# Kernel optimization log

Measured on AMD Instinct MI355X. Metric: run time of the kernel, lower is better.

Reference implementation:

```python
import jax, jax.numpy as jnp
import numpy as np

WS = (8, 8, 8)          # window_size (d, h, w) -- all equal
N_TOK = WS[0] * WS[1] * WS[2]   # 512
DIM = 192
HEADS = 6
HEAD_DIM = DIM // HEADS  # 32
B_ = 64                  # num_windows * batch (batch = 1)


def _build_rel_coords_table():
    # matches torch: meshgrid of arange(-(w-1), w) per axis, normalized, *8, signed log2
    r = np.arange(-(WS[0] - 1), WS[0], dtype=np.float32)
    tab = np.stack(np.meshgrid(r, r, r, indexing='ij'), axis=-1)[None]  # (1,15,15,15,3)
    tab = tab / (WS[0] - 1)
    tab = tab * 8.0
    tab = np.sign(tab) * np.log2(np.abs(tab) + 1.0) / np.log2(8.0)
    return tab.astype(np.float32)


def _build_rel_pos_index():
    c = np.arange(WS[0])
    coords = np.stack(np.meshgrid(c, c, c, indexing='ij'))          # (3, 8, 8, 8)
    flat = coords.reshape(3, -1)                                     # (3, N)
    rel = flat[:, :, None] - flat[:, None, :]                        # (3, N, N)
    rel = rel.transpose(1, 2, 0).copy()                              # (N, N, 3)
    rel += WS[0] - 1
    rel[:, :, 0] *= (2 * WS[1] - 1) * (2 * WS[2] - 1)
    rel[:, :, 1] *= 2 * WS[2] - 1
    return rel.sum(-1).astype(np.int32)                              # (N, N)


def setup_inputs() -> dict:
    key = jax.random.key(0)
    ks = jax.random.split(key, 8)
    x = jax.random.normal(ks[0], (B_, N_TOK, DIM), dtype=jnp.float32)
    # 0 / -inf style additive mask (use large negative finite for stability)
    m = jax.random.uniform(ks[1], (B_, N_TOK, N_TOK))
    mask = jnp.where(m < 0.1, jnp.float32(-1e4), jnp.float32(0.0))
    w_qkv = jax.random.normal(ks[2], (3 * DIM, DIM), dtype=jnp.float32) * (DIM ** -0.5)
    q_bias = jnp.zeros((DIM,), jnp.float32)
    v_bias = jnp.zeros((DIM,), jnp.float32)
    cpb_w1 = jax.random.normal(ks[3], (512, 3), dtype=jnp.float32) * 0.3
    cpb_b1 = jnp.zeros((512,), jnp.float32)
    cpb_w2 = jax.random.normal(ks[4], (HEADS, 512), dtype=jnp.float32) * 0.05
    rel_coords_table = jnp.asarray(_build_rel_coords_table())
    rel_pos_index = jnp.asarray(_build_rel_pos_index())
    return {"x": x, "mask": mask, "w_qkv": w_qkv, "q_bias": q_bias,
            "v_bias": v_bias, "cpb_w1": cpb_w1, "cpb_b1": cpb_b1,
            "cpb_w2": cpb_w2, "rel_coords_table": rel_coords_table,
            "rel_pos_index": rel_pos_index}


def reference(x, mask, w_qkv, q_bias, v_bias, cpb_w1, cpb_b1, cpb_w2,
              rel_coords_table, rel_pos_index):
    Bw, N, C = x.shape
    H, D = HEADS, HEAD_DIM
    # qkv projection with bias = cat(q_bias, zeros, v_bias)
    qkv_bias = jnp.concatenate([q_bias, jnp.zeros_like(v_bias), v_bias])
    qkv = x @ w_qkv.T + qkv_bias                       # (Bw, N, 3C)
    qkv = qkv.reshape(Bw, N, 3, H, D).transpose(2, 0, 3, 1, 4)
    q, k, v = qkv[0], qkv[1], qkv[2]                   # (Bw, H, N, D)
    # continuous position bias MLP: 3 -> 512 -> H
    tab = rel_coords_table.reshape(-1, 3)              # (3375, 3)
    tab = jax.nn.relu(tab @ cpb_w1.T + cpb_b1) @ cpb_w2.T  # (3375, H)
    bias = tab[rel_pos_index.reshape(-1)].reshape(N, N, H)
    bias = 16.0 * jax.nn.sigmoid(bias.transpose(2, 0, 1))  # (H, N, N)
    # SDPA with additive mask (standard 1/sqrt(D) scaling, as in forward_flash)
    scale = jnp.float32(1.0 / np.sqrt(D))
    scores = jnp.einsum('bhnd,bhmd->bhnm', q, k) * scale
    scores = scores + mask[:, None, :, :] + bias[None]
    attn = jax.nn.softmax(scores, axis=-1)
    out = jnp.einsum('bhnm,bhmd->bhnd', attn, v)       # (Bw, H, N, D)
    return out
```

## Files before the change

kernel.cpp:

```cpp
#include <hip/hip_runtime.h>
#include <hip/hip_bf16.h>


typedef __bf16 bf16x8 __attribute__((ext_vector_type(8)));
typedef __bf16 bf16x4v __attribute__((ext_vector_type(4)));
typedef float  f32x4  __attribute__((ext_vector_type(4)));
typedef _Float16 f16x4 __attribute__((ext_vector_type(4)));
typedef _Float16 f16x8 __attribute__((ext_vector_type(8)));
typedef unsigned uint2v __attribute__((ext_vector_type(2)));
typedef int int4v __attribute__((ext_vector_type(4)));
typedef unsigned long long u64;

#define LOG2E 1.4426950408889634f

__device__ __forceinline__ bf16x8 cvt2_bf16x8(f32x4 a, f32x4 b) {
  bf16x8 r;
  r[0] = (__bf16)a[0]; r[1] = (__bf16)a[1]; r[2] = (__bf16)a[2]; r[3] = (__bf16)a[3];
  r[4] = (__bf16)b[0]; r[5] = (__bf16)b[1]; r[6] = (__bf16)b[2]; r[7] = (__bf16)b[3];
  return r;
}

__device__ __forceinline__ unsigned pack2bf(float a, float b) {
  unsigned short ua = __builtin_bit_cast(unsigned short, (__bf16)a);
  unsigned short ub = __builtin_bit_cast(unsigned short, (__bf16)b);
  return (unsigned)ua | ((unsigned)ub << 16);
}

__device__ __forceinline__ bf16x8 frag_from_words(unsigned w0, unsigned w1,
                                                  unsigned w2, unsigned w3) {
  union { unsigned u[4]; bf16x8 v; } f;
  f.u[0] = w0; f.u[1] = w1; f.u[2] = w2; f.u[3] = w3;
  return f.v;
}

#define PREP_MB    2048
#define PREP_WCONV 108
#define PREP_CPB   3375
#define PREP_GRID  (PREP_MB + PREP_WCONV + PREP_CPB)

__global__ __launch_bounds__(256) void prep_kernel(
    const float* __restrict__ w, __bf16* __restrict__ wbf,
    const float* __restrict__ table, const float* __restrict__ w1,
    const float* __restrict__ b1, const float* __restrict__ w2,
    float* __restrict__ tab6,
    const float* __restrict__ m, u64* __restrict__ bits)
{
  __shared__ float red[4][6];
  int blk = blockIdx.x;
  if (blk < PREP_MB) {
    int li8 = threadIdx.x & 7;
    for (size_t t = (size_t)blk * 256 + threadIdx.x;
         t < 2097152ull; t += (size_t)PREP_MB * 256) {
      const float* mp = m + t * 8;
      f32x4 v0 = *(const f32x4*)mp;
      f32x4 v1 = *(const f32x4*)(mp + 4);
      unsigned byte =
          (v0[0] == 0.f ? 1u : 0u)  | (v0[1] == 0.f ? 2u : 0u) |
          (v0[2] == 0.f ? 4u : 0u)  | (v0[3] == 0.f ? 8u : 0u) |
          (v1[0] == 0.f ? 16u : 0u) | (v1[1] == 0.f ? 32u : 0u) |
          (v1[2] == 0.f ? 64u : 0u) | (v1[3] == 0.f ? 128u : 0u);
      u64 part = (u64)byte << (8 * li8);
      part |= __shfl_xor(part, 1);
      part |= __shfl_xor(part, 2);
      part |= __shfl_xor(part, 4);
      if (li8 == 0) {
        int w_ = (int)(t >> 3);
        int b = w_ >> 12, i = (w_ >> 3) & 511, jw = w_ & 7;
        bits[(((size_t)b * 8 + jw) << 9) + i] = part;
      }
    }
  } else if (blk < PREP_MB + PREP_WCONV) {
    int t = (blk - PREP_MB) * 256 + threadIdx.x;
    f32x4 v = *(const f32x4*)(w + (size_t)t * 4);
    bf16x4v o;
    o[0] = (__bf16)v[0]; o[1] = (__bf16)v[1]; o[2] = (__bf16)v[2]; o[3] = (__bf16)v[3];
    *(bf16x4v*)(wbf + (size_t)t * 4) = o;
  } else {
    int p = blk - PREP_MB - PREP_WCONV;
    float c0 = table[p * 3 + 0], c1 = table[p * 3 + 1], c2 = table[p * 3 + 2];
    float acc[6] = {0.f, 0.f, 0.f, 0.f, 0.f, 0.f};
#pragma unroll
    for (int jj = 0; jj < 2; ++jj) {
      int j = threadIdx.x + jj * 256;
      float hv = w1[j * 3 + 0] * c0 + w1[j * 3 + 1] * c1 + w1[j * 3 + 2] * c2 + b1[j];
      hv = fmaxf(hv, 0.0f);
#pragma unroll
      for (int t = 0; t < 6; ++t) acc[t] += w2[t * 512 + j] * hv;
    }
#pragma unroll
    for (int t = 0; t < 6; ++t) {
      acc[t] += __shfl_xor(acc[t], 1);
      acc[t] += __shfl_xor(acc[t], 2);
      acc[t] += __shfl_xor(acc[t], 4);
      acc[t] += __shfl_xor(acc[t], 8);
      acc[t] += __shfl_xor(acc[t], 16);
      acc[t] += __shfl_xor(acc[t], 32);
    }
    int wave = threadIdx.x >> 6;
    if ((threadIdx.x & 63) == 0)
#pragma unroll
      for (int t = 0; t < 6; ++t) red[wave][t] = acc[t];
    __syncthreads();
    if (threadIdx.x < 6) {
      int t = threadIdx.x;
      float s = red[0][t] + red[1][t] + red[2][t] + red[3][t];
      float sig = 16.0f / (1.0f + expf(-s));
      tab6[p * 8 + t] = sig * LOG2E;
    }
  }
}

__global__ __launch_bounds__(256) void bias_kernel(
    const int* __restrict__ relidx,
    const float* __restrict__ tab6,
    _Float16* __restrict__ biasH)
{
  int q4 = blockIdx.x * 256 + threadIdx.x;
  int ij = q4 * 4;
  int i = ij >> 9, p = ij & 511;
  int jblk = p >> 6, g = (p >> 4) & 3, kf = (p >> 2) & 3;
  int j = (jblk << 6) + kf * 16 + g * 4;
  int4v idx4 = *(const int4v*)(relidx + (i << 9) + j);
  float val[6][4];
#pragma unroll
  for (int u = 0; u < 4; ++u) {
    f32x4 lo = *(const f32x4*)(tab6 + (size_t)idx4[u] * 8);
    f32x4 hi = *(const f32x4*)(tab6 + (size_t)idx4[u] * 8 + 4);
    val[0][u] = lo[0]; val[1][u] = lo[1]; val[2][u] = lo[2];
    val[3][u] = lo[3]; val[4][u] = hi[0]; val[5][u] = hi[1];
  }
#pragma unroll
  for (int t6 = 0; t6 < 6; ++t6) {
    f16x4 o = {(_Float16)val[t6][0], (_Float16)val[t6][1],
               (_Float16)val[t6][2], (_Float16)val[t6][3]};
    *(f16x4*)(biasH + (size_t)t6 * 262144 + ij) = o;
  }
}

#define FUSED_GRID 384

__global__ __launch_bounds__(512, 2) void fused_kernel(
    const float* __restrict__ x,
    const __bf16* __restrict__ wbf,
    const float* __restrict__ qb,
    const float* __restrict__ vb,
    const u64* __restrict__ bits,
    const _Float16* __restrict__ biasH,
    float* __restrict__ out)
{
  __shared__ __bf16 Qs[512][40];
  __shared__ __bf16 Ks[512][40];
  __shared__ __bf16 Vs[32][520];

  int blk = blockIdx.x;
  int xcd = blk & 7, seq = blk >> 3;
  int h = seq >> 3;
  int b = xcd * 8 + (seq & 7);
  int lane = threadIdx.x & 63, wave = threadIdx.x >> 6;
  int g = lane >> 4, li = lane & 15;
  int bh = b * 6 + h;
  int gsh = 4 * g;
  const float CQ = 0.17677669529663687f * LOG2E;

  {
    const __bf16* wp[6];
    float bb[6];
#pragma unroll
    for (int n = 0; n < 6; ++n) {
      int wcol, reg = n >> 1, sub = n & 1;
      int d = sub * 16 + li;
      wcol = reg * 192 + h * 32 + d;
      wp[n] = wbf + (size_t)wcol * 192 + 8 * g;
      bb[n] = (reg == 0) ? qb[wcol] : (reg == 2 ? vb[h * 32 + d] : 0.0f);
    }
#pragma unroll
    for (int mi = 0; mi < 2; ++mi) {
      int rowb = wave * 64 + mi * 32;
      bf16x8 a[2][6];
#pragma unroll
      for (int mm = 0; mm < 2; ++mm)
#pragma unroll
        for (int k = 0; k < 6; ++k) {
          const float* xp = x + (size_t)(b * 512 + rowb + mm * 16 + li) * 192 + k * 32 + 8 * g;
          f32x4 x0 = *(const f32x4*)xp;
          f32x4 x1 = *(const f32x4*)(xp + 4);
          a[mm][k] = cvt2_bf16x8(x0, x1);
        }
      f32x4 acc[2][6];
#pragma unroll
      for (int n = 0; n < 6; ++n) {
        f32x4 v = {bb[n], bb[n], bb[n], bb[n]};
        acc[0][n] = v; acc[1][n] = v;
      }
#pragma unroll
      for (int k = 0; k < 6; ++k)
#pragma unroll
        for (int n = 0; n < 6; ++n) {
          bf16x8 bf = *(const bf16x8*)(wp[n] + k * 32);
          acc[0][n] = __builtin_amdgcn_mfma_f32_16x16x32_bf16(a[0][k], bf, acc[0][n], 0, 0, 0);
          acc[1][n] = __builtin_amdgcn_mfma_f32_16x16x32_bf16(a[1][k], bf, acc[1][n], 0, 0, 0);
        }
#pragma unroll
      for (int mm = 0; mm < 2; ++mm) {
        int tok0 = rowb + mm * 16 + 4 * g;
#pragma unroll
        for (int n = 0; n < 2; ++n)
#pragma unroll
          for (int t = 0; t < 4; ++t)
            Qs[tok0 + t][n * 16 + li] = (__bf16)(acc[mm][n][t] * CQ);
#pragma unroll
        for (int n = 2; n < 4; ++n)
#pragma unroll
          for (int t = 0; t < 4; ++t)
            Ks[tok0 + t][(n - 2) * 16 + li] = (__bf16)acc[mm][n][t];
#pragma unroll
        for (int n = 4; n < 6; ++n) {
          bf16x4v pk;
#pragma unroll
          for (int t = 0; t < 4; ++t) pk[t] = (__bf16)acc[mm][n][t];
          *(bf16x4v*)&Vs[(n - 4) * 16 + li][tok0] = pk;
        }
      }
    }
  }
  __syncthreads();

  int qbase = wave * 64;
  const _Float16* biasb = biasH + (size_t)h * 262144 + g * 16;
  const u64* bitsb = bits + (size_t)b * 4096;

  bf16x8 qfrag[4];
#pragma unroll
  for (int qf = 0; qf < 4; ++qf)
    qfrag[qf] = *(const bf16x8*)&Qs[qbase + qf * 16 + li][8 * g];

  union { unsigned short us[8]; bf16x8 v; } onesu;
#pragma unroll
  for (int i = 0; i < 8; ++i) onesu.us[i] = 0x3F80;
  bf16x8 ones = onesu.v;

  f32x4 oacc[4][2] = {};
  f32x4 lacc[4] = {};

  for (int kb = 0; kb < 8; ++kb) {
    int j64 = kb * 64;
    unsigned mbl[4], mbh[4];
#pragma unroll
    for (int qf = 0; qf < 4; ++qf) {
      u64 m64 = bitsb[(kb << 9) + qbase + qf * 16 + li] >> gsh;
      mbl[qf] = (unsigned)m64;
      mbh[qf] = (unsigned)(m64 >> 32);
    }
    bf16x8 kfr[4];
#pragma unroll
    for (int kf = 0; kf < 4; ++kf)
      kfr[kf] = *(const bf16x8*)&Ks[j64 + kf * 16 + li][8 * g];
    bf16x8 vfr[2][2];
#pragma unroll
    for (int df = 0; df < 2; ++df)
#pragma unroll
      for (int c = 0; c < 2; ++c)
        vfr[df][c] = *(const bf16x8*)&Vs[df * 16 + li][j64 + c * 32 + 8 * g];
    f16x8 hv8[4][2];
#pragma unroll
    for (int qf = 0; qf < 4; ++qf) {
      const _Float16* bp = biasb + (qbase + qf * 16 + li) * 512 + j64;
      hv8[qf][0] = *(const f16x8*)(bp);
      hv8[qf][1] = *(const f16x8*)(bp + 8);
    }

    __builtin_amdgcn_s_setprio(1);
#pragma unroll
    for (int c = 0; c < 2; ++c) {
      unsigned lo[4][2], hi[4][2];
#pragma unroll
      for (int kfl = 0; kfl < 2; ++kfl) {
        int kf = c * 2 + kfl;
        const int hsel = kf >> 1, hoff = (kf & 1) * 4;
        const int bb0 = (kf & 1) * 16;
#pragma unroll
        for (int qf = 0; qf < 4; ++qf) {
          f16x8 hb = hv8[qf][hsel];
          f32x4 ci = {(float)hb[hoff], (float)hb[hoff + 1],
                      (float)hb[hoff + 2], (float)hb[hoff + 3]};
          f32x4 s = __builtin_amdgcn_mfma_f32_16x16x32_bf16(kfr[kf], qfrag[qf], ci, 0, 0, 0);
          unsigned mword = hsel ? mbh[qf] : mbl[qf];
          unsigned m0 = (unsigned)((int)(mword << (31 - (bb0 + 0))) >> 31);
          unsigned m1 = (unsigned)((int)(mword << (31 - (bb0 + 1))) >> 31);
          unsigned m2 = (unsigned)((int)(mword << (31 - (bb0 + 2))) >> 31);
          unsigned m3 = (unsigned)((int)(mword << (31 - (bb0 + 3))) >> 31);
          float p0 = __builtin_bit_cast(float,
              __builtin_bit_cast(unsigned, __builtin_amdgcn_exp2f(s[0])) & m0);
          float p1 = __builtin_bit_cast(float,
              __builtin_bit_cast(unsigned, __builtin_amdgcn_exp2f(s[1])) & m1);
          float p2 = __builtin_bit_cast(float,
              __builtin_bit_cast(unsigned, __builtin_amdgcn_exp2f(s[2])) & m2);
          float p3 = __builtin_bit_cast(float,
              __builtin_bit_cast(unsigned, __builtin_amdgcn_exp2f(s[3])) & m3);
          lo[qf][kfl] = pack2bf(p0, p1);
          hi[qf][kfl] = pack2bf(p2, p3);
        }
      }
#pragma unroll
      for (int qf = 0; qf < 4; ++qf) {
        uint2v sl = __builtin_amdgcn_permlane32_swap(lo[qf][0], lo[qf][1], 0, 0);
        uint2v wl = __builtin_amdgcn_permlane16_swap(sl.x, sl.y, 0, 0);
        uint2v sh = __builtin_amdgcn_permlane32_swap(hi[qf][0], hi[qf][1], 0, 0);
        uint2v wh = __builtin_amdgcn_permlane16_swap(sh.x, sh.y, 0, 0);
        bf16x8 pf = frag_from_words(wl.x, wh.x, wl.y, wh.y);
        oacc[qf][0] = __builtin_amdgcn_mfma_f32_16x16x32_bf16(vfr[0][c], pf, oacc[qf][0], 0, 0, 0);
        oacc[qf][1] = __builtin_amdgcn_mfma_f32_16x16x32_bf16(vfr[1][c], pf, oacc[qf][1], 0, 0, 0);
        lacc[qf]    = __builtin_amdgcn_mfma_f32_16x16x32_bf16(ones, pf, lacc[qf], 0, 0, 0);
      }
    }
    __builtin_amdgcn_s_setprio(0);
  }

#pragma unroll
  for (int qf = 0; qf < 4; ++qf) {
    float linv = 1.0f / lacc[qf][0];
#pragma unroll
    for (int df = 0; df < 2; ++df) {
      float* op = out + ((size_t)bh * 512 + qbase + qf * 16 + li) * 32 + df * 16 + 4 * g;
      f32x4 r2 = oacc[qf][df] * linv;
      *(f32x4*)op = r2;
    }
  }
}

extern "C" void kernel_launch(void* const* d_in, const int* in_sizes, int n_in,
                              void* d_out, int out_size, void* d_ws, size_t ws_size,
                              hipStream_t stream) {
  const float* x    = (const float*)d_in[0];
  const float* mask = (const float*)d_in[1];
  const float* wqkv = (const float*)d_in[2];
  const float* qb   = (const float*)d_in[3];
  const float* vb   = (const float*)d_in[4];
  const float* w1   = (const float*)d_in[5];
  const float* b1   = (const float*)d_in[6];
  const float* w2   = (const float*)d_in[7];
  const float* tbl  = (const float*)d_in[8];
  const int*   ridx = (const int*)d_in[9];
  float* out = (float*)d_out;

  char* ws = (char*)d_ws;
  float*    tab6  = (float*)(ws);
  _Float16* biasH = (_Float16*)(ws + 131072);
  u64*      bits  = (u64*)(ws + 131072 + 3145728);
  __bf16*   wbf   = (__bf16*)(ws + 131072 + 3145728 + 2097152);

  prep_kernel<<<PREP_GRID, 256, 0, stream>>>(wqkv, wbf, tbl, w1, b1, w2, tab6,
                                             mask, bits);
  bias_kernel<<<256, 256, 0, stream>>>(ridx, tab6, biasH);
  fused_kernel<<<FUSED_GRID, 512, 0, stream>>>(x, wbf, qb, vb, bits, biasH, out);
}
```

Before: 122.2 us.

## Share one LDS buffer for Q and K by splitting the QKV projection

Merges the separate Q and K shared-memory tiles into one buffer. The projection is split into two passes: the first computes Q and V, and each wave reads its Q fragments into registers. After a barrier, the second pass reloads x and computes K into the same buffer. This cuts LDS per block by about 40KB so more blocks can fit per CU, at the cost of reading x twice, converting it twice and adding an extra __syncthreads.

```diff
diff --git a/kernel.cpp b/kernel.cpp
--- a/kernel.cpp
+++ b/kernel.cpp
@@ -148,8 +148,7 @@
     const _Float16* __restrict__ biasH,
     float* __restrict__ out)
 {
-  __shared__ __bf16 Qs[512][40];
-  __shared__ __bf16 Ks[512][40];
+  __shared__ __bf16 KQs[512][40];
   __shared__ __bf16 Vs[32][520];
 
   int blk = blockIdx.x;
@@ -162,77 +161,111 @@
   int gsh = 4 * g;
   const float CQ = 0.17677669529663687f * LOG2E;
 
-  {
-    const __bf16* wp[6];
-    float bb[6];
-#pragma unroll
-    for (int n = 0; n < 6; ++n) {
-      int wcol, reg = n >> 1, sub = n & 1;
-      int d = sub * 16 + li;
-      wcol = reg * 192 + h * 32 + d;
-      wp[n] = wbf + (size_t)wcol * 192 + 8 * g;
-      bb[n] = (reg == 0) ? qb[wcol] : (reg == 2 ? vb[h * 32 + d] : 0.0f);
-    }
-#pragma unroll
-    for (int mi = 0; mi < 2; ++mi) {
-      int rowb = wave * 64 + mi * 32;
-      bf16x8 a[2][6];
-#pragma unroll
-      for (int mm = 0; mm < 2; ++mm)
-#pragma unroll
-        for (int k = 0; k < 6; ++k) {
-          const float* xp = x + (size_t)(b * 512 + rowb + mm * 16 + li) * 192 + k * 32 + 8 * g;
-          f32x4 x0 = *(const f32x4*)xp;
-          f32x4 x1 = *(const f32x4*)(xp + 4);
-          a[mm][k] = cvt2_bf16x8(x0, x1);
-        }
-      f32x4 acc[2][6];
-#pragma unroll
-      for (int n = 0; n < 6; ++n) {
-        f32x4 v = {bb[n], bb[n], bb[n], bb[n]};
-        acc[0][n] = v; acc[1][n] = v;
-      }
-#pragma unroll
-      for (int k = 0; k < 6; ++k)
-#pragma unroll
-        for (int n = 0; n < 6; ++n) {
-          bf16x8 bf = *(const bf16x8*)(wp[n] + k * 32);
-          acc[0][n] = __builtin_amdgcn_mfma_f32_16x16x32_bf16(a[0][k], bf, acc[0][n], 0, 0, 0);
-          acc[1][n] = __builtin_amdgcn_mfma_f32_16x16x32_bf16(a[1][k], bf, acc[1][n], 0, 0, 0);
-        }
-#pragma unroll
-      for (int mm = 0; mm < 2; ++mm) {
-        int tok0 = rowb + mm * 16 + 4 * g;
-#pragma unroll
-        for (int n = 0; n < 2; ++n)
-#pragma unroll
-          for (int t = 0; t < 4; ++t)
-            Qs[tok0 + t][n * 16 + li] = (__bf16)(acc[mm][n][t] * CQ);
-#pragma unroll
-        for (int n = 2; n < 4; ++n)
-#pragma unroll
-          for (int t = 0; t < 4; ++t)
-            Ks[tok0 + t][(n - 2) * 16 + li] = (__bf16)acc[mm][n][t];
-#pragma unroll
-        for (int n = 4; n < 6; ++n) {
-          bf16x4v pk;
-#pragma unroll
-          for (int t = 0; t < 4; ++t) pk[t] = (__bf16)acc[mm][n][t];
-          *(bf16x4v*)&Vs[(n - 4) * 16 + li][tok0] = pk;
-        }
-      }
-    }
-  }
+  const __bf16* wp[6];
+  float bbv[6];
+#pragma unroll
+  for (int n = 0; n < 6; ++n) {
+    int reg = n >> 1, sub = n & 1;
+    int d = sub * 16 + li;
+    int wcol = reg * 192 + h * 32 + d;
+    wp[n] = wbf + (size_t)wcol * 192 + 8 * g;
+    bbv[n] = (reg == 0) ? qb[wcol] : (reg == 2 ? vb[h * 32 + d] : 0.0f);
+  }
+
+#pragma unroll
+  for (int mi = 0; mi < 2; ++mi) {
+    int rowb = wave * 64 + mi * 32;
+    bf16x8 a[2][6];
+#pragma unroll
+    for (int mm = 0; mm < 2; ++mm)
+#pragma unroll
+      for (int k = 0; k < 6; ++k) {
+        const float* xp = x + (size_t)(b * 512 + rowb + mm * 16 + li) * 192 + k * 32 + 8 * g;
+        f32x4 x0 = *(const f32x4*)xp;
+        f32x4 x1 = *(const f32x4*)(xp + 4);
+        a[mm][k] = cvt2_bf16x8(x0, x1);
+      }
+    f32x4 acc[2][4];
+#pragma unroll
+    for (int u = 0; u < 2; ++u) {
+      f32x4 vq = {bbv[u], bbv[u], bbv[u], bbv[u]};
+      f32x4 vv = {bbv[4 + u], bbv[4 + u], bbv[4 + u], bbv[4 + u]};
+      acc[0][u] = vq; acc[1][u] = vq;
+      acc[0][2 + u] = vv; acc[1][2 + u] = vv;
+    }
+#pragma unroll
+    for (int k = 0; k < 6; ++k) {
+#pragma unroll
+      for (int u = 0; u < 2; ++u) {
+        bf16x8 bq = *(const bf16x8*)(wp[u] + k * 32);
+        bf16x8 bv = *(const bf16x8*)(wp[4 + u] + k * 32);
+        acc[0][u]     = __builtin_amdgcn_mfma_f32_16x16x32_bf16(a[0][k], bq, acc[0][u], 0, 0, 0);
+        acc[1][u]     = __builtin_amdgcn_mfma_f32_16x16x32_bf16(a[1][k], bq, acc[1][u], 0, 0, 0);
+        acc[0][2 + u] = __builtin_amdgcn_mfma_f32_16x16x32_bf16(a[0][k], bv, acc[0][2 + u], 0, 0, 0);
+        acc[1][2 + u] = __builtin_amdgcn_mfma_f32_16x16x32_bf16(a[1][k], bv, acc[1][2 + u], 0, 0, 0);
+      }
+    }
+#pragma unroll
+    for (int mm = 0; mm < 2; ++mm) {
+      int tok0 = rowb + mm * 16 + 4 * g;
+#pragma unroll
+      for (int u = 0; u < 2; ++u)
+#pragma unroll
+        for (int t = 0; t < 4; ++t)
+          KQs[tok0 + t][u * 16 + li] = (__bf16)(acc[mm][u][t] * CQ);
+#pragma unroll
+      for (int u = 0; u < 2; ++u) {
+        bf16x4v pk;
+#pragma unroll
+        for (int t = 0; t < 4; ++t) pk[t] = (__bf16)acc[mm][2 + u][t];
+        *(bf16x4v*)&Vs[u * 16 + li][tok0] = pk;
+      }
+    }
+  }
+
+  int qbase = wave * 64;
+  bf16x8 qfrag[4];
+#pragma unroll
+  for (int qf = 0; qf < 4; ++qf)
+    qfrag[qf] = *(const bf16x8*)&KQs[qbase + qf * 16 + li][8 * g];
   __syncthreads();
 
-  int qbase = wave * 64;
+#pragma unroll
+  for (int mi = 0; mi < 2; ++mi) {
+    int rowb = wave * 64 + mi * 32;
+    bf16x8 a[2][6];
+#pragma unroll
+    for (int mm = 0; mm < 2; ++mm)
+#pragma unroll
+      for (int k = 0; k < 6; ++k) {
+        const float* xp = x + (size_t)(b * 512 + rowb + mm * 16 + li) * 192 + k * 32 + 8 * g;
+        f32x4 x0 = *(const f32x4*)xp;
+        f32x4 x1 = *(const f32x4*)(xp + 4);
+        a[mm][k] = cvt2_bf16x8(x0, x1);
+      }
+    f32x4 acc[2][2] = {};
+#pragma unroll
+    for (int k = 0; k < 6; ++k)
+#pragma unroll
+      for (int u = 0; u < 2; ++u) {
+        bf16x8 bk = *(const bf16x8*)(wp[2 + u] + k * 32);
+        acc[0][u] = __builtin_amdgcn_mfma_f32_16x16x32_bf16(a[0][k], bk, acc[0][u], 0, 0, 0);
+        acc[1][u] = __builtin_amdgcn_mfma_f32_16x16x32_bf16(a[1][k], bk, acc[1][u], 0, 0, 0);
+      }
+#pragma unroll
+    for (int mm = 0; mm < 2; ++mm) {
+      int tok0 = rowb + mm * 16 + 4 * g;
+#pragma unroll
+      for (int u = 0; u < 2; ++u)
+#pragma unroll
+        for (int t = 0; t < 4; ++t)
+          KQs[tok0 + t][u * 16 + li] = (__bf16)acc[mm][u][t];
+    }
+  }
+  __syncthreads();
+
   const _Float16* biasb = biasH + (size_t)h * 262144 + g * 16;
   const u64* bitsb = bits + (size_t)b * 4096;
-
-  bf16x8 qfrag[4];
-#pragma unroll
-  for (int qf = 0; qf < 4; ++qf)
-    qfrag[qf] = *(const bf16x8*)&Qs[qbase + qf * 16 + li][8 * g];
 
   union { unsigned short us[8]; bf16x8 v; } onesu;
 #pragma unroll
@@ -254,7 +287,7 @@
     bf16x8 kfr[4];
 #pragma unroll
     for (int kf = 0; kf < 4; ++kf)
-      kfr[kf] = *(const bf16x8*)&Ks[j64 + kf * 16 + li][8 * g];
+      kfr[kf] = *(const bf16x8*)&KQs[j64 + kf * 16 + li][8 * g];
     bf16x8 vfr[2][2];
 #pragma unroll
     for (int df = 0; df < 2; ++df)
```

Result: slower. 133.8 us (+9.5%).
